# Performance work log

Hardware: AMD Instinct MI355X
Metric: run time of the kernel (lower is better)

Reference implementation:

```python
import jax, jax.numpy as jnp
import numpy as np

B, F, T = 8, 128, 16384

def setup_inputs() -> dict:
    key = jax.random.key(0)
    data = jax.random.uniform(key, (B, F, T), dtype=jnp.float32)  # non-negative spectrogram magnitudes
    return {
        "data": data,
        "alpha": jnp.float32(0.98),
        "r": jnp.float32(0.5),
        "delta": jnp.float32(2.0),
        "s": jnp.float32(0.5),
        "eps": jnp.float32(1e-6),
    }

def reference(data, alpha, r, delta, s, eps):
    # Faithful to source: EMA smoother M is built from batch element 0 only,
    # m[:, 0] = s * x[:, 0]; m[:, j] = (1-s) * m[:, j-1] + s * x[:, j]
    x0 = data[0]  # [F, T]

    def step(m, xt):  # m: [F], xt: [F]
        m = (1.0 - s) * m + s * xt
        return m, m

    init = jnp.zeros((F,), dtype=data.dtype)
    _, M = jax.lax.scan(step, init, x0.T)  # M: [T, F]
    M = M.T  # [F, T], broadcasts against data [B, F, T]

    Madde = M + eps
    Mepow = jnp.sign(Madde) * jnp.power(jnp.abs(Madde), alpha)
    EonM = data / Mepow
    r_abs = jnp.abs(r)
    pcen = jnp.power(EonM + delta, r_abs) - jnp.power(delta, r_abs)
    return pcen
```

## Files before the change

### kernel.cpp

```cpp
#include <hip/hip_runtime.h>
#include <math.h>

#define B_DIM 8
#define F_DIM 128
#define T_DIM 16384

#define SCAN_THREADS 512
#define CHUNK (T_DIM / SCAN_THREADS)
#define CHUNK4 (CHUNK / 4)
#define LOG2_CHUNK 5

#define MV (F_DIM * T_DIM / 4)
#define APPLY_THREADS 256

typedef float f32x4 __attribute__((ext_vector_type(4)));

__global__ __launch_bounds__(SCAN_THREADS) void pcen_scan_kernel(
    const float* __restrict__ x0,
    const float* __restrict__ p_alpha,
    const float* __restrict__ p_s,
    const float* __restrict__ p_eps,
    float* __restrict__ mepow)
{
    const float alpha = p_alpha[0];
    const float s     = p_s[0];
    const float eps   = p_eps[0];
    const float a     = 1.0f - s;

    const int f    = blockIdx.x;
    const int tid  = threadIdx.x;
    const int lane = tid & 63;
    const int wave = tid >> 6;

    const f32x4* xrow = (const f32x4*)(x0 + (size_t)f * T_DIM);
    f32x4*       mrow = (f32x4*)(mepow + (size_t)f * T_DIM);

    const int vbase = tid * CHUNK4;

    f32x4 y[CHUNK4];
    float m = 0.0f;
#pragma unroll
    for (int j = 0; j < CHUNK4; ++j) {
        f32x4 x = xrow[vbase + j];
        m = fmaf(a, m, s * x.x); x.x = m;
        m = fmaf(a, m, s * x.y); x.y = m;
        m = fmaf(a, m, s * x.z); x.z = m;
        m = fmaf(a, m, s * x.w); x.w = m;
        y[j] = x;
    }

    float A = a;
#pragma unroll
    for (int i = 0; i < LOG2_CHUNK; ++i) A = A * A;
    float B = m;

#pragma unroll
    for (int d = 1; d < 64; d <<= 1) {
        float Ap = __shfl_up(A, d);
        float Bp = __shfl_up(B, d);
        if (lane >= d) {
            B = fmaf(A, Bp, B);
            A = A * Ap;
        }
    }

    __shared__ float wA[SCAN_THREADS / 64];
    __shared__ float wB[SCAN_THREADS / 64];
    if (lane == 63) { wA[wave] = A; wB[wave] = B; }
    __syncthreads();

    float Ae = __shfl_up(A, 1);
    float Be = __shfl_up(B, 1);
    if (lane == 0) { Ae = 1.0f; Be = 0.0f; }

    float cB = 0.0f;
    for (int w = 0; w < wave; ++w) cB = fmaf(wA[w], cB, wB[w]);

    const float m_in = fmaf(Ae, cB, Be);

    float ap = a;
#pragma unroll
    for (int j = 0; j < CHUNK4; ++j) {
        f32x4 yv = y[j];
        f32x4 o;
        {
            float mv = fmaf(ap, m_in, yv.x); ap *= a;
            float mad = mv + eps;
            o.x = copysignf(__builtin_amdgcn_exp2f(alpha * __builtin_amdgcn_logf(fabsf(mad))), mad);
        }
        {
            float mv = fmaf(ap, m_in, yv.y); ap *= a;
            float mad = mv + eps;
            o.y = copysignf(__builtin_amdgcn_exp2f(alpha * __builtin_amdgcn_logf(fabsf(mad))), mad);
        }
        {
            float mv = fmaf(ap, m_in, yv.z); ap *= a;
            float mad = mv + eps;
            o.z = copysignf(__builtin_amdgcn_exp2f(alpha * __builtin_amdgcn_logf(fabsf(mad))), mad);
        }
        {
            float mv = fmaf(ap, m_in, yv.w); ap *= a;
            float mad = mv + eps;
            o.w = copysignf(__builtin_amdgcn_exp2f(alpha * __builtin_amdgcn_logf(fabsf(mad))), mad);
        }
        mrow[vbase + j] = o;
    }
}

__global__ __launch_bounds__(APPLY_THREADS) void pcen_apply_kernel(
    const float* __restrict__ data,
    const float* __restrict__ mepow,
    const float* __restrict__ p_r,
    const float* __restrict__ p_delta,
    float* __restrict__ out)
{
    const float r_abs = fabsf(p_r[0]);
    const float delta = p_delta[0];

    const int v = blockIdx.x * APPLY_THREADS + threadIdx.x;

    const f32x4* __restrict__ d4 = (const f32x4*)data + v;
    const f32x4* __restrict__ m4 = (const f32x4*)mepow + v;
    f32x4* __restrict__       o4 = (f32x4*)out + v;

    const f32x4 mp = *m4;
    f32x4 rc;
    rc.x = 1.0f / mp.x;
    rc.y = 1.0f / mp.y;
    rc.z = 1.0f / mp.z;
    rc.w = 1.0f / mp.w;

    if (r_abs == 0.5f) {
        const float dpr = sqrtf(delta);
#pragma unroll
        for (int b = 0; b < B_DIM; ++b) {
            f32x4 x = __builtin_nontemporal_load(d4 + b * MV);
            f32x4 o;
            o.x = sqrtf(fmaf(x.x, rc.x, delta)) - dpr;
            o.y = sqrtf(fmaf(x.y, rc.y, delta)) - dpr;
            o.z = sqrtf(fmaf(x.z, rc.z, delta)) - dpr;
            o.w = sqrtf(fmaf(x.w, rc.w, delta)) - dpr;
            __builtin_nontemporal_store(o, o4 + b * MV);
        }
    } else {
        const float dpr = powf(delta, r_abs);
#pragma unroll
        for (int b = 0; b < B_DIM; ++b) {
            f32x4 x = __builtin_nontemporal_load(d4 + b * MV);
            f32x4 o;
            o.x = powf(fmaf(x.x, rc.x, delta), r_abs) - dpr;
            o.y = powf(fmaf(x.y, rc.y, delta), r_abs) - dpr;
            o.z = powf(fmaf(x.z, rc.z, delta), r_abs) - dpr;
            o.w = powf(fmaf(x.w, rc.w, delta), r_abs) - dpr;
            __builtin_nontemporal_store(o, o4 + b * MV);
        }
    }
}

extern "C" void kernel_launch(void* const* d_in, const int* in_sizes, int n_in,
                              void* d_out, int out_size, void* d_ws, size_t ws_size,
                              hipStream_t stream) {
    const float* data    = (const float*)d_in[0];
    const float* p_alpha = (const float*)d_in[1];
    const float* p_r     = (const float*)d_in[2];
    const float* p_delta = (const float*)d_in[3];
    const float* p_s     = (const float*)d_in[4];
    const float* p_eps   = (const float*)d_in[5];
    float* out = (float*)d_out;

    float* mepow = (float*)d_ws;

    pcen_scan_kernel<<<F_DIM, SCAN_THREADS, 0, stream>>>(
        data, p_alpha, p_s, p_eps, mepow);

    pcen_apply_kernel<<<MV / APPLY_THREADS, APPLY_THREADS, 0, stream>>>(
        data, mepow, p_r, p_delta, out);
}
```

Measured before the change: 136.1 us.

## Fuse EMA scan and PCEN apply into one kernel with redundant per-block scans

Merges the scan kernel and the apply kernel into a single launch. Each block recomputes the EMA scan of batch 0 for one frequency row, keeps the reciprocal of M^alpha in registers, and then applies PCEN to two batch elements for that row. This removes the workspace write and re-read of the mepow intermediate and one kernel launch. In exchange, the scan and its transcendental work is done four times per row, and the apply phase now has long per-thread strided chunks instead of fully coalesced vector accesses.

```diff
diff --git a/kernel.cpp b/kernel.cpp
--- a/kernel.cpp
+++ b/kernel.cpp
@@ -5,36 +5,41 @@
 #define F_DIM 128
 #define T_DIM 16384
 
-#define SCAN_THREADS 512
-#define CHUNK (T_DIM / SCAN_THREADS)
+#define THREADS 512
+#define CHUNK  (T_DIM / THREADS)
 #define CHUNK4 (CHUNK / 4)
 #define LOG2_CHUNK 5
 
-#define MV (F_DIM * T_DIM / 4)
-#define APPLY_THREADS 256
+#define BATCHES_PER_BLOCK 2
+#define BLOCKS_PER_F (B_DIM / BATCHES_PER_BLOCK)
+#define GRID (F_DIM * BLOCKS_PER_F)
 
 typedef float f32x4 __attribute__((ext_vector_type(4)));
 
-__global__ __launch_bounds__(SCAN_THREADS) void pcen_scan_kernel(
-    const float* __restrict__ x0,
+__global__ __launch_bounds__(THREADS, 4) void pcen_fused_kernel(
+    const float* __restrict__ data,
     const float* __restrict__ p_alpha,
+    const float* __restrict__ p_r,
+    const float* __restrict__ p_delta,
     const float* __restrict__ p_s,
     const float* __restrict__ p_eps,
-    float* __restrict__ mepow)
+    float* __restrict__ out)
 {
     const float alpha = p_alpha[0];
     const float s     = p_s[0];
     const float eps   = p_eps[0];
     const float a     = 1.0f - s;
+    const float r_abs = fabsf(p_r[0]);
+    const float delta = p_delta[0];
 
-    const int f    = blockIdx.x;
+    const int bid  = blockIdx.x;
+    const int f    = bid & (F_DIM - 1);
+    const int sub  = bid >> 7;
     const int tid  = threadIdx.x;
     const int lane = tid & 63;
     const int wave = tid >> 6;
 
-    const f32x4* xrow = (const f32x4*)(x0 + (size_t)f * T_DIM);
-    f32x4*       mrow = (f32x4*)(mepow + (size_t)f * T_DIM);
-
+    const f32x4* xrow = (const f32x4*)(data + (size_t)f * T_DIM);
     const int vbase = tid * CHUNK4;
 
     f32x4 y[CHUNK4];
@@ -64,8 +69,8 @@
         }
     }
 
-    __shared__ float wA[SCAN_THREADS / 64];
-    __shared__ float wB[SCAN_THREADS / 64];
+    __shared__ float wA[THREADS / 64];
+    __shared__ float wB[THREADS / 64];
     if (lane == 63) { wA[wave] = A; wB[wave] = B; }
     __syncthreads();
 
@@ -82,77 +87,75 @@
 #pragma unroll
     for (int j = 0; j < CHUNK4; ++j) {
         f32x4 yv = y[j];
-        f32x4 o;
+        f32x4 me;
         {
             float mv = fmaf(ap, m_in, yv.x); ap *= a;
             float mad = mv + eps;
-            o.x = copysignf(__builtin_amdgcn_exp2f(alpha * __builtin_amdgcn_logf(fabsf(mad))), mad);
+            me.x = copysignf(__builtin_amdgcn_exp2f(alpha * __builtin_amdgcn_logf(fabsf(mad))), mad);
         }
         {
             float mv = fmaf(ap, m_in, yv.y); ap *= a;
             float mad = mv + eps;
-            o.y = copysignf(__builtin_amdgcn_exp2f(alpha * __builtin_amdgcn_logf(fabsf(mad))), mad);
+            me.y = copysignf(__builtin_amdgcn_exp2f(alpha * __builtin_amdgcn_logf(fabsf(mad))), mad);
         }
         {
             float mv = fmaf(ap, m_in, yv.z); ap *= a;
             float mad = mv + eps;
-            o.z = copysignf(__builtin_amdgcn_exp2f(alpha * __builtin_amdgcn_logf(fabsf(mad))), mad);
+            me.z = copysignf(__builtin_amdgcn_exp2f(alpha * __builtin_amdgcn_logf(fabsf(mad))), mad);
         }
         {
             float mv = fmaf(ap, m_in, yv.w); ap *= a;
             float mad = mv + eps;
-            o.w = copysignf(__builtin_amdgcn_exp2f(alpha * __builtin_amdgcn_logf(fabsf(mad))), mad);
+            me.w = copysignf(__builtin_amdgcn_exp2f(alpha * __builtin_amdgcn_logf(fabsf(mad))), mad);
         }
-        mrow[vbase + j] = o;
+        f32x4 rc;
+        rc.x = 1.0f / me.x;
+        rc.y = 1.0f / me.y;
+        rc.z = 1.0f / me.z;
+        rc.w = 1.0f / me.w;
+        y[j] = rc;
     }
-}
 
-__global__ __launch_bounds__(APPLY_THREADS) void pcen_apply_kernel(
-    const float* __restrict__ data,
-    const float* __restrict__ mepow,
-    const float* __restrict__ p_r,
-    const float* __restrict__ p_delta,
-    float* __restrict__ out)
-{
-    const float r_abs = fabsf(p_r[0]);
-    const float delta = p_delta[0];
-
-    const int v = blockIdx.x * APPLY_THREADS + threadIdx.x;
-
-    const f32x4* __restrict__ d4 = (const f32x4*)data + v;
-    const f32x4* __restrict__ m4 = (const f32x4*)mepow + v;
-    f32x4* __restrict__       o4 = (f32x4*)out + v;
-
-    const f32x4 mp = *m4;
-    f32x4 rc;
-    rc.x = 1.0f / mp.x;
-    rc.y = 1.0f / mp.y;
-    rc.z = 1.0f / mp.z;
-    rc.w = 1.0f / mp.w;
+    const size_t row_off = (size_t)f * T_DIM;
+    const int b0 = sub * BATCHES_PER_BLOCK;
 
     if (r_abs == 0.5f) {
         const float dpr = sqrtf(delta);
 #pragma unroll
-        for (int b = 0; b < B_DIM; ++b) {
-            f32x4 x = __builtin_nontemporal_load(d4 + b * MV);
-            f32x4 o;
-            o.x = sqrtf(fmaf(x.x, rc.x, delta)) - dpr;
-            o.y = sqrtf(fmaf(x.y, rc.y, delta)) - dpr;
-            o.z = sqrtf(fmaf(x.z, rc.z, delta)) - dpr;
-            o.w = sqrtf(fmaf(x.w, rc.w, delta)) - dpr;
-            __builtin_nontemporal_store(o, o4 + b * MV);
+        for (int bb = 0; bb < BATCHES_PER_BLOCK; ++bb) {
+            const int b = b0 + bb;
+            const f32x4* __restrict__ d4 = (const f32x4*)(data + (size_t)b * F_DIM * T_DIM + row_off) + vbase;
+            f32x4* __restrict__       o4 = (f32x4*)(out + (size_t)b * F_DIM * T_DIM + row_off) + vbase;
+#pragma unroll
+            for (int j = 0; j < CHUNK4; ++j) {
+                f32x4 x = __builtin_nontemporal_load(d4 + j);
+                f32x4 rc = y[j];
+                f32x4 o;
+                o.x = sqrtf(fmaf(x.x, rc.x, delta)) - dpr;
+                o.y = sqrtf(fmaf(x.y, rc.y, delta)) - dpr;
+                o.z = sqrtf(fmaf(x.z, rc.z, delta)) - dpr;
+                o.w = sqrtf(fmaf(x.w, rc.w, delta)) - dpr;
+                __builtin_nontemporal_store(o, o4 + j);
+            }
         }
     } else {
         const float dpr = powf(delta, r_abs);
 #pragma unroll
-        for (int b = 0; b < B_DIM; ++b) {
-            f32x4 x = __builtin_nontemporal_load(d4 + b * MV);
-            f32x4 o;
-            o.x = powf(fmaf(x.x, rc.x, delta), r_abs) - dpr;
-            o.y = powf(fmaf(x.y, rc.y, delta), r_abs) - dpr;
-            o.z = powf(fmaf(x.z, rc.z, delta), r_abs) - dpr;
-            o.w = powf(fmaf(x.w, rc.w, delta), r_abs) - dpr;
-            __builtin_nontemporal_store(o, o4 + b * MV);
+        for (int bb = 0; bb < BATCHES_PER_BLOCK; ++bb) {
+            const int b = b0 + bb;
+            const f32x4* __restrict__ d4 = (const f32x4*)(data + (size_t)b * F_DIM * T_DIM + row_off) + vbase;
+            f32x4* __restrict__       o4 = (f32x4*)(out + (size_t)b * F_DIM * T_DIM + row_off) + vbase;
+#pragma unroll
+            for (int j = 0; j < CHUNK4; ++j) {
+                f32x4 x = __builtin_nontemporal_load(d4 + j);
+                f32x4 rc = y[j];
+                f32x4 o;
+                o.x = powf(fmaf(x.x, rc.x, delta), r_abs) - dpr;
+                o.y = powf(fmaf(x.y, rc.y, delta), r_abs) - dpr;
+                o.z = powf(fmaf(x.z, rc.z, delta), r_abs) - dpr;
+                o.w = powf(fmaf(x.w, rc.w, delta), r_abs) - dpr;
+                __builtin_nontemporal_store(o, o4 + j);
+            }
         }
     }
 }
@@ -168,11 +171,6 @@
     const float* p_eps   = (const float*)d_in[5];
     float* out = (float*)d_out;
 
-    float* mepow = (float*)d_ws;
-
-    pcen_scan_kernel<<<F_DIM, SCAN_THREADS, 0, stream>>>(
-        data, p_alpha, p_s, p_eps, mepow);
-
-    pcen_apply_kernel<<<MV / APPLY_THREADS, APPLY_THREADS, 0, stream>>>(
-        data, mepow, p_r, p_delta, out);
+    pcen_fused_kernel<<<GRID, THREADS, 0, stream>>>(
+        data, p_alpha, p_r, p_delta, p_s, p_eps, out);
 }
```

Measured after the change: 290.0 us. 113% more time.
